# Performance work log

Hardware: AMD Instinct MI355X
Metric: run time of the kernel (lower is better)

The kernel has to match this reference:

```python
import jax, jax.numpy as jnp
import numpy as np

N_NODES = 50000
N_EDGES = 800000
IN_CH = 96
HID = 128
OUT_CH = 2


def _glorot(key, shape):
    lim = 1.0 / np.sqrt(shape[0])
    return jax.random.uniform(key, shape, jnp.float32, -lim, lim)


def setup_inputs() -> dict:
    key = jax.random.key(0)
    ks = jax.random.split(key, 16)
    x = jax.random.normal(ks[0], (N_NODES, IN_CH), jnp.float32)
    edge_index = jax.random.randint(ks[1], (2, N_EDGES), 0, N_NODES, jnp.int64)
    dims = [(IN_CH, HID), (HID, HID), (HID, HID // 2)]
    params = {}
    for i, (di, do) in enumerate(dims, start=1):
        params[f"Wl{i}"] = _glorot(ks[2 * i], (di, do))      # neighbor (lin_l)
        params[f"Wr{i}"] = _glorot(ks[2 * i + 1], (di, do))  # root (lin_r)
        params[f"b{i}"] = jnp.zeros((do,), jnp.float32)
    params["Wc"] = _glorot(ks[10], (HID // 2, OUT_CH))
    params["bc"] = jnp.zeros((OUT_CH,), jnp.float32)
    return {"x": x, "edge_index": edge_index, **params}


def _sage_conv(x, src, dst, Wl, Wr, b):
    # scatter-mean of source-node features into destination nodes (PyG mean aggr)
    n = x.shape[0]
    agg = jax.ops.segment_sum(x[src], dst, num_segments=n)          # [N, d]
    cnt = jax.ops.segment_sum(jnp.ones((src.shape[0], 1), x.dtype), dst, num_segments=n)
    mean = agg / jnp.maximum(cnt, 1.0)
    return mean @ Wl + x @ Wr + b


def reference(x, edge_index, Wl1, Wr1, b1, Wl2, Wr2, b2, Wl3, Wr3, b3, Wc, bc):
    src, dst = edge_index[0], edge_index[1]
    h = jax.nn.relu(_sage_conv(x, src, dst, Wl1, Wr1, b1))
    h = jax.nn.relu(_sage_conv(h, src, dst, Wl2, Wr2, b2))
    h = jax.nn.relu(_sage_conv(h, src, dst, Wl3, Wr3, b3))
    return h @ Wc + bc  # [N, 2] logits (dropout is identity at inference)
```

## Files before the change

kernel.cpp:

```cpp
#include <hip/hip_runtime.h>

#define N_NODES 50000
#define N_EDGES 800000
#define SCAN_NB ((N_NODES + 255) / 256)

#define NB_E 128
#define CH (N_EDGES / NB_E)
#define RSZ 25000
#define HALF_WORDS (RSZ / 2)

#define CVT_ITEMS  (N_NODES * 96 / 4)
#define CVT_NB  ((CVT_ITEMS + 255) / 256)
#define PACK1_NB 12
#define PACK2_NB 16
#define PACK3_NB 8
#define PREP_NB (CVT_NB + PACK1_NB + PACK2_NB + PACK3_NB)

typedef __attribute__((ext_vector_type(8))) short short8;
typedef __attribute__((ext_vector_type(8))) unsigned short ushort8;
typedef __attribute__((ext_vector_type(4))) float f32x4;

__device__ __forceinline__ float bf2f(unsigned short u) {
  unsigned int x = ((unsigned int)u) << 16;
  return __builtin_bit_cast(float, x);
}
__device__ __forceinline__ unsigned short f2bf(float f) {
  unsigned int x = __builtin_bit_cast(unsigned int, f);
  unsigned int r = x + 0x7FFFu + ((x >> 16) & 1u);
  return (unsigned short)(r >> 16);
}


__device__ __forceinline__ void pack_w_section(const float* __restrict__ Wl,
                                               const float* __restrict__ Wr,
                                               ushort* __restrict__ wcat,
                                               int K, int J2, int bid) {
  int idx = bid * 256 + threadIdx.x;
  int Jcat = 2 * J2;
  int total = (K / 8) * Jcat;
  if (idx >= total) return;
  int kk8 = idx / Jcat, j = idx % Jcat;
  const float* W = (j < J2) ? Wl : Wr;
  int jj = (j < J2) ? j : j - J2;
  ushort8 v;
  #pragma unroll
  for (int i = 0; i < 8; i++) v[i] = f2bf(W[(kk8 * 8 + i) * J2 + jj]);
  *(ushort8*)(wcat + (size_t)idx * 8) = v;
}

__global__ __launch_bounds__(256) void prep_kernel(
    const float* __restrict__ x, ushort* __restrict__ xb,
    const float* __restrict__ Wl1, const float* __restrict__ Wr1, ushort* __restrict__ wcat1,
    const float* __restrict__ Wl2, const float* __restrict__ Wr2, ushort* __restrict__ wcat2,
    const float* __restrict__ Wl3, const float* __restrict__ Wr3, ushort* __restrict__ wcat3) {
  int bid = blockIdx.x;
  if (bid < CVT_NB) {
    int i = bid * 256 + threadIdx.x;
    if (i < CVT_ITEMS) {
      f32x4 v = __builtin_nontemporal_load((const f32x4*)(x + i * 4));
      ushort4 o = make_ushort4(f2bf(v.x), f2bf(v.y), f2bf(v.z), f2bf(v.w));
      *(ushort4*)(xb + i * 4) = o;
    }
    return;
  }
  bid -= CVT_NB;
  if (bid < PACK1_NB) { pack_w_section(Wl1, Wr1, wcat1, 96, 128, bid); return; }
  bid -= PACK1_NB;
  if (bid < PACK2_NB) { pack_w_section(Wl2, Wr2, wcat2, 128, 128, bid); return; }
  bid -= PACK2_NB;
  pack_w_section(Wl3, Wr3, wcat3, 128, 64, bid);
}


__global__ __launch_bounds__(256) void hist_lds(const int* __restrict__ dst,
                                                ushort* __restrict__ hist_g) {
  __shared__ unsigned hist[HALF_WORDS];
  for (int j = threadIdx.x; j < HALF_WORDS; j += 256) hist[j] = 0;
  __syncthreads();
  int b = blockIdx.x >> 1, r = blockIdx.x & 1;
  int base = b * CH;
  for (int i = threadIdx.x; i < CH; i += 256) {
    int d = __builtin_nontemporal_load(dst + base + i);
    unsigned ld = (unsigned)(d - r * RSZ);
    if (ld < RSZ) atomicAdd(&hist[ld >> 1], (ld & 1) ? 65536u : 1u);
  }
  __syncthreads();
  unsigned* outp = (unsigned*)(hist_g + (size_t)b * N_NODES + r * RSZ);
  for (int j = threadIdx.x; j < HALF_WORDS; j += 256) outp[j] = hist[j];
}

__device__ __forceinline__ int block_excl_scan_256(int v, int tid, int* tot_out) {
  __shared__ int ws[4];
  int lane = tid & 63, wid = tid >> 6;
  int incl = v;
  #pragma unroll
  for (int off = 1; off < 64; off <<= 1) {
    int t = __shfl_up(incl, off);
    if (lane >= off) incl += t;
  }
  if (lane == 63) ws[wid] = incl;
  __syncthreads();
  int woff = 0;
  #pragma unroll
  for (int w = 0; w < 4; w++) woff += (w < wid) ? ws[w] : 0;
  *tot_out = ws[0] + ws[1] + ws[2] + ws[3];
  return woff + incl - v;
}

__global__ __launch_bounds__(256) void scanA(const ushort* __restrict__ hist_g,
                                             ushort* __restrict__ cum_g,
                                             int* __restrict__ rowptr,
                                             int* __restrict__ blocksum, int n) {
  int i = blockIdx.x * 256 + threadIdx.x;
  int run = 0;
  if (i < n) {
    for (int b = 0; b < NB_E; b++) {
      size_t o = (size_t)b * N_NODES + i;
      int c = hist_g[o];
      cum_g[o] = (ushort)run;
      run += c;
    }
  }
  int tot;
  int excl = block_excl_scan_256(run, threadIdx.x, &tot);
  if (i < n) rowptr[i] = excl;
  if (threadIdx.x == 0) blocksum[blockIdx.x] = tot;
}

__global__ __launch_bounds__(256) void scanB(const int* __restrict__ blocksum,
                                             int* __restrict__ blockoff,
                                             int* __restrict__ rowptr, int nb, int n) {
  int tid = threadIdx.x;
  int v = (tid < nb) ? blocksum[tid] : 0;
  int tot;
  int excl = block_excl_scan_256(v, tid, &tot);
  if (tid < nb) blockoff[tid] = excl;
  if (tid == 0) rowptr[n] = tot;
}

__global__ __launch_bounds__(256) void scanC(int* __restrict__ rowptr,
                                             const int* __restrict__ blockoff, int n) {
  int i = blockIdx.x * 256 + threadIdx.x;
  if (i < n) rowptr[i] += blockoff[blockIdx.x];
}

__global__ __launch_bounds__(256) void fill_lds(const int* __restrict__ src,
                                                const int* __restrict__ dst,
                                                const ushort* __restrict__ cum_g,
                                                const int* __restrict__ rowptr,
                                                ushort* __restrict__ csr) {
  __shared__ unsigned cur[HALF_WORDS];
  int b = blockIdx.x >> 1, r = blockIdx.x & 1;
  const unsigned* cg = (const unsigned*)(cum_g + (size_t)b * N_NODES + r * RSZ);
  for (int j = threadIdx.x; j < HALF_WORDS; j += 256) cur[j] = cg[j];
  __syncthreads();
  int base = b * CH;
  for (int i = threadIdx.x; i < CH; i += 256) {
    int d = __builtin_nontemporal_load(dst + base + i);
    int s = __builtin_nontemporal_load(src + base + i);
    unsigned ld = (unsigned)(d - r * RSZ);
    if (ld < RSZ) {
      unsigned old = atomicAdd(&cur[ld >> 1], (ld & 1) ? 65536u : 1u);
      unsigned loc = (ld & 1) ? (old >> 16) : (old & 0xffffu);
      csr[(size_t)rowptr[d] + loc] = (ushort)s;
    }
  }
}

template <int K, int J2>
__global__ __launch_bounds__(256) void gemm_mfma(
    const ushort* __restrict__ hb, const ushort* __restrict__ wcat,
    ushort* __restrict__ tl, ushort* __restrict__ tr, int n) {
  constexpr int Jcat = 2 * J2;
  constexpr int NT = Jcat / 16;
  constexpr int KS = K / 32;
  constexpr int BM = 128;
  constexpr int LDS_US = (BM * Jcat > K * Jcat) ? BM * Jcat : K * Jcat;
  __shared__ ushort lds[LDS_US];

  int tid = threadIdx.x;
  int wid = tid >> 6, lane = tid & 63;
  int row0 = blockIdx.x * BM;

  constexpr int WCH = K * Jcat / 8;
  for (int c = tid; c < WCH; c += 256) {
    *(ushort8*)(lds + c * 8) = *(const ushort8*)(wcat + (size_t)c * 8);
  }
  __syncthreads();

  int rg = lane >> 4, lc = lane & 15;
  int r0 = row0 + wid * 32 + lc;
  int r1 = r0 + 16;
  long ar0 = (long)min(r0, n - 1) * K;
  long ar1 = (long)min(r1, n - 1) * K;

  f32x4 acc[2][NT];
  #pragma unroll
  for (int mt = 0; mt < 2; mt++)
    #pragma unroll
    for (int jt = 0; jt < NT; jt++) acc[mt][jt] = (f32x4){0.f, 0.f, 0.f, 0.f};

  #pragma unroll
  for (int ks = 0; ks < KS; ks++) {
    int koff = ks * 32 + rg * 8;
    short8 a0 = *(const short8*)(hb + ar0 + koff);
    short8 a1 = *(const short8*)(hb + ar1 + koff);
    int kk8 = ks * 4 + rg;
    #pragma unroll
    for (int jt = 0; jt < NT; jt++) {
      short8 bfr = *(const short8*)(lds + ((size_t)kk8 * Jcat + jt * 16 + lc) * 8);
      acc[0][jt] = __builtin_amdgcn_mfma_f32_16x16x32_bf16(a0, bfr, acc[0][jt], 0, 0, 0);
      acc[1][jt] = __builtin_amdgcn_mfma_f32_16x16x32_bf16(a1, bfr, acc[1][jt], 0, 0, 0);
    }
  }
  __syncthreads();

  #pragma unroll
  for (int mt = 0; mt < 2; mt++) {
    int rbase = wid * 32 + mt * 16 + rg * 4;
    #pragma unroll
    for (int jt = 0; jt < NT; jt++) {
      int col = jt * 16 + lc;
      #pragma unroll
      for (int r = 0; r < 4; r++)
        lds[(size_t)(rbase + r) * Jcat + col] = f2bf(acc[mt][jt][r]);
    }
  }
  __syncthreads();

  constexpr int CPR = J2 / 8;
  for (int i = tid; i < BM * 2 * CPR; i += 256) {
    int row = i / (2 * CPR), cc = i % (2 * CPR);
    int grow = row0 + row;
    if (grow < n) {
      ushort8 v = *(ushort8*)(lds + (size_t)row * Jcat + cc * 8);
      ushort* dstp = (cc < CPR) ? (tl + (size_t)grow * J2 + cc * 8)
                                : (tr + (size_t)grow * J2 + (size_t)(cc - CPR) * 8);
      *(ushort8*)dstp = v;
    }
  }
}

__global__ __launch_bounds__(256) void agg_relu128(
    const ushort* __restrict__ tl, const ushort* __restrict__ tr,
    const float* __restrict__ bias,
    const int* __restrict__ rowptr, const ushort* __restrict__ csr,
    ushort* __restrict__ hout, int n) {
  int node = blockIdx.x * 16 + (threadIdx.x >> 4);
  int lane = threadIdx.x & 15;
  if (node >= n) return;
  int lo = rowptr[node], hi = rowptr[node + 1];

  float s[8];
  #pragma unroll
  for (int i = 0; i < 8; i++) s[i] = 0.f;

  int e = lo;
  for (; e + 1 < hi; e += 2) {
    int i0 = csr[e], i1 = csr[e + 1];
    ushort8 v0 = *(const ushort8*)(tl + (size_t)i0 * 128 + lane * 8);
    ushort8 v1 = *(const ushort8*)(tl + (size_t)i1 * 128 + lane * 8);
    #pragma unroll
    for (int i = 0; i < 8; i++) s[i] += bf2f(v0[i]) + bf2f(v1[i]);
  }
  if (e < hi) {
    int i0 = csr[e];
    ushort8 v0 = *(const ushort8*)(tl + (size_t)i0 * 128 + lane * 8);
    #pragma unroll
    for (int i = 0; i < 8; i++) s[i] += bf2f(v0[i]);
  }

  int deg = hi - lo;
  float inv = (deg > 0) ? 1.f / (float)deg : 0.f;
  ushort8 tv = *(const ushort8*)(tr + (size_t)node * 128 + lane * 8);
  float4 b0 = *(const float4*)(bias + lane * 8);
  float4 b1 = *(const float4*)(bias + lane * 8 + 4);
  float bb[8] = {b0.x, b0.y, b0.z, b0.w, b1.x, b1.y, b1.z, b1.w};
  ushort8 o;
  #pragma unroll
  for (int i = 0; i < 8; i++) {
    float v = s[i] * inv + bf2f(tv[i]) + bb[i];
    o[i] = f2bf(v > 0.f ? v : 0.f);
  }
  *(ushort8*)(hout + (size_t)node * 128 + lane * 8) = o;
}

__global__ __launch_bounds__(256) void agg_head(
    const ushort* __restrict__ tl, const ushort* __restrict__ tr,
    const float* __restrict__ bias, const float* __restrict__ Wc,
    const float* __restrict__ bc,
    const int* __restrict__ rowptr, const ushort* __restrict__ csr,
    float* __restrict__ out, int n) {
  int node = blockIdx.x * 32 + (threadIdx.x >> 3);
  int lane = threadIdx.x & 7;
  if (node >= n) return;
  int lo = rowptr[node], hi = rowptr[node + 1];

  float s[8];
  #pragma unroll
  for (int i = 0; i < 8; i++) s[i] = 0.f;

  int e = lo;
  for (; e + 1 < hi; e += 2) {
    int i0 = csr[e], i1 = csr[e + 1];
    ushort8 v0 = *(const ushort8*)(tl + (size_t)i0 * 64 + lane * 8);
    ushort8 v1 = *(const ushort8*)(tl + (size_t)i1 * 64 + lane * 8);
    #pragma unroll
    for (int i = 0; i < 8; i++) s[i] += bf2f(v0[i]) + bf2f(v1[i]);
  }
  if (e < hi) {
    int i0 = csr[e];
    ushort8 v0 = *(const ushort8*)(tl + (size_t)i0 * 64 + lane * 8);
    #pragma unroll
    for (int i = 0; i < 8; i++) s[i] += bf2f(v0[i]);
  }

  int deg = hi - lo;
  float inv = (deg > 0) ? 1.f / (float)deg : 0.f;
  ushort8 tv = *(const ushort8*)(tr + (size_t)node * 64 + lane * 8);
  float p0 = 0.f, p1 = 0.f;
  #pragma unroll
  for (int i = 0; i < 8; i++) {
    int k = lane * 8 + i;
    float v = s[i] * inv + bf2f(tv[i]) + bias[k];
    v = v > 0.f ? v : 0.f;
    p0 += v * Wc[k * 2 + 0];
    p1 += v * Wc[k * 2 + 1];
  }
  #pragma unroll
  for (int off = 1; off < 8; off <<= 1) {
    p0 += __shfl_xor(p0, off);
    p1 += __shfl_xor(p1, off);
  }
  if (lane == 0) {
    out[(size_t)node * 2 + 0] = p0 + bc[0];
    out[(size_t)node * 2 + 1] = p1 + bc[1];
  }
}

extern "C" void kernel_launch(void* const* d_in, const int* in_sizes, int n_in,
                              void* d_out, int out_size, void* d_ws, size_t ws_size,
                              hipStream_t stream) {
  const float* x   = (const float*)d_in[0];
  const int*   ei  = (const int*)d_in[1];
  const float* Wl1 = (const float*)d_in[2];
  const float* Wr1 = (const float*)d_in[3];
  const float* b1  = (const float*)d_in[4];
  const float* Wl2 = (const float*)d_in[5];
  const float* Wr2 = (const float*)d_in[6];
  const float* b2  = (const float*)d_in[7];
  const float* Wl3 = (const float*)d_in[8];
  const float* Wr3 = (const float*)d_in[9];
  const float* b3  = (const float*)d_in[10];
  const float* Wc  = (const float*)d_in[11];
  const float* bc  = (const float*)d_in[12];
  float* out = (float*)d_out;

  const int* src = ei;
  const int* dst = ei + N_EDGES;

  char* ws = (char*)d_ws;
  size_t off = 0;
  auto alloc = [&](size_t bytes) -> void* {
    void* p = ws + off;
    off += (bytes + 255) & ~(size_t)255;
    return p;
  };
  int*    rowptr   = (int*)alloc((N_NODES + 1) * sizeof(int));
  ushort* csr      = (ushort*)alloc(N_EDGES * sizeof(ushort));
  int*    blocksum = (int*)alloc(256 * sizeof(int));
  int*    blockoff = (int*)alloc(256 * sizeof(int));
  ushort* xb       = (ushort*)alloc((size_t)N_NODES * 96 * 2);
  ushort* wcat1    = (ushort*)alloc((size_t)96 * 256 * 2);
  ushort* wcat2    = (ushort*)alloc((size_t)128 * 256 * 2);
  ushort* wcat3    = (ushort*)alloc((size_t)128 * 128 * 2);
  ushort* tl       = (ushort*)alloc((size_t)N_NODES * 128 * 2);
  ushort* tr       = (ushort*)alloc((size_t)N_NODES * 128 * 2);
  ushort* hA       = (ushort*)alloc((size_t)N_NODES * 128 * 2);
  ushort* hB       = (ushort*)alloc((size_t)N_NODES * 128 * 2);
  (void)ws_size; (void)n_in; (void)in_sizes; (void)out_size;

  ushort* hist_g = tl;
  ushort* cum_g  = tr;

  prep_kernel<<<PREP_NB, 256, 0, stream>>>(x, xb,
                                           Wl1, Wr1, wcat1,
                                           Wl2, Wr2, wcat2,
                                           Wl3, Wr3, wcat3);

  hist_lds<<<NB_E * 2, 256, 0, stream>>>(dst, hist_g);
  scanA<<<SCAN_NB, 256, 0, stream>>>(hist_g, cum_g, rowptr, blocksum, N_NODES);
  scanB<<<1, 256, 0, stream>>>(blocksum, blockoff, rowptr, SCAN_NB, N_NODES);
  scanC<<<SCAN_NB, 256, 0, stream>>>(rowptr, blockoff, N_NODES);
  fill_lds<<<NB_E * 2, 256, 0, stream>>>(src, dst, cum_g, rowptr, csr);

  const int gemm_grid = (N_NODES + 127) / 128;
  const int agg_grid  = (N_NODES + 15) / 16;
  const int head_grid = (N_NODES + 31) / 32;

  gemm_mfma<96, 128><<<gemm_grid, 256, 0, stream>>>(xb, wcat1, tl, tr, N_NODES);
  agg_relu128<<<agg_grid, 256, 0, stream>>>(tl, tr, b1, rowptr, csr, hA, N_NODES);
  gemm_mfma<128, 128><<<gemm_grid, 256, 0, stream>>>(hA, wcat2, tl, tr, N_NODES);
  agg_relu128<<<agg_grid, 256, 0, stream>>>(tl, tr, b2, rowptr, csr, hB, N_NODES);
  gemm_mfma<128, 64><<<gemm_grid, 256, 0, stream>>>(hB, wcat3, tl, tr, N_NODES);
  agg_head<<<head_grid, 256, 0, stream>>>(tl, tr, b3, Wc, bc, rowptr, csr, out, N_NODES);
}
```

Baseline: 195.3 us.

## Fuse scan passes, read GEMM weights from global, unroll gather by eight

Merges the two small scan kernels into one, where each block recomputes the block-offset scan and applies its own offset, removing a launch. The GEMM no longer stages weights in LDS and writes outputs straight from the accumulators with scalar stores, dropping barriers and the staging pass at the cost of uncoalesced 2-byte stores and repeated global/L2 weight reads. The aggregation kernels add an eight-edge unrolled gather so more neighbour loads are in flight at once.

```diff
diff --git a/kernel.cpp b/kernel.cpp
--- a/kernel.cpp
+++ b/kernel.cpp
@@ -127,21 +127,19 @@
   if (threadIdx.x == 0) blocksum[blockIdx.x] = tot;
 }
 
-__global__ __launch_bounds__(256) void scanB(const int* __restrict__ blocksum,
-                                             int* __restrict__ blockoff,
-                                             int* __restrict__ rowptr, int nb, int n) {
+__global__ __launch_bounds__(256) void scanBC(const int* __restrict__ blocksum,
+                                              int* __restrict__ rowptr, int n) {
+  __shared__ int exls[256];
   int tid = threadIdx.x;
-  int v = (tid < nb) ? blocksum[tid] : 0;
+  int v = (tid < SCAN_NB) ? blocksum[tid] : 0;
   int tot;
   int excl = block_excl_scan_256(v, tid, &tot);
-  if (tid < nb) blockoff[tid] = excl;
-  if (tid == 0) rowptr[n] = tot;
-}
-
-__global__ __launch_bounds__(256) void scanC(int* __restrict__ rowptr,
-                                             const int* __restrict__ blockoff, int n) {
-  int i = blockIdx.x * 256 + threadIdx.x;
-  if (i < n) rowptr[i] += blockoff[blockIdx.x];
+  exls[tid] = excl;
+  __syncthreads();
+  int myoff = exls[blockIdx.x];
+  int i = blockIdx.x * 256 + tid;
+  if (i < n) rowptr[i] += myoff;
+  if (blockIdx.x == 0 && tid == 0) rowptr[n] = tot;
 }
 
 __global__ __launch_bounds__(256) void fill_lds(const int* __restrict__ src,
@@ -174,21 +172,11 @@
   constexpr int Jcat = 2 * J2;
   constexpr int NT = Jcat / 16;
   constexpr int KS = K / 32;
-  constexpr int BM = 128;
-  constexpr int LDS_US = (BM * Jcat > K * Jcat) ? BM * Jcat : K * Jcat;
-  __shared__ ushort lds[LDS_US];
 
   int tid = threadIdx.x;
   int wid = tid >> 6, lane = tid & 63;
-  int row0 = blockIdx.x * BM;
-
-  constexpr int WCH = K * Jcat / 8;
-  for (int c = tid; c < WCH; c += 256) {
-    *(ushort8*)(lds + c * 8) = *(const ushort8*)(wcat + (size_t)c * 8);
-  }
-  __syncthreads();
-
   int rg = lane >> 4, lc = lane & 15;
+  int row0 = blockIdx.x * 128;
   int r0 = row0 + wid * 32 + lc;
   int r1 = r0 + 16;
   long ar0 = (long)min(r0, n - 1) * K;
@@ -208,12 +196,11 @@
     int kk8 = ks * 4 + rg;
     #pragma unroll
     for (int jt = 0; jt < NT; jt++) {
-      short8 bfr = *(const short8*)(lds + ((size_t)kk8 * Jcat + jt * 16 + lc) * 8);
+      short8 bfr = *(const short8*)(wcat + ((size_t)kk8 * Jcat + jt * 16 + lc) * 8);
       acc[0][jt] = __builtin_amdgcn_mfma_f32_16x16x32_bf16(a0, bfr, acc[0][jt], 0, 0, 0);
       acc[1][jt] = __builtin_amdgcn_mfma_f32_16x16x32_bf16(a1, bfr, acc[1][jt], 0, 0, 0);
     }
   }
-  __syncthreads();
 
   #pragma unroll
   for (int mt = 0; mt < 2; mt++) {
@@ -221,22 +208,13 @@
     #pragma unroll
     for (int jt = 0; jt < NT; jt++) {
       int col = jt * 16 + lc;
+      ushort* outp = (col < J2) ? tl : tr;
+      int cm = (col < J2) ? col : col - J2;
       #pragma unroll
-      for (int r = 0; r < 4; r++)
-        lds[(size_t)(rbase + r) * Jcat + col] = f2bf(acc[mt][jt][r]);
-    }
-  }
-  __syncthreads();
-
-  constexpr int CPR = J2 / 8;
-  for (int i = tid; i < BM * 2 * CPR; i += 256) {
-    int row = i / (2 * CPR), cc = i % (2 * CPR);
-    int grow = row0 + row;
-    if (grow < n) {
-      ushort8 v = *(ushort8*)(lds + (size_t)row * Jcat + cc * 8);
-      ushort* dstp = (cc < CPR) ? (tl + (size_t)grow * J2 + cc * 8)
-                                : (tr + (size_t)grow * J2 + (size_t)(cc - CPR) * 8);
-      *(ushort8*)dstp = v;
+      for (int r = 0; r < 4; r++) {
+        int grow = row0 + rbase + r;
+        if (grow < n) outp[(size_t)grow * J2 + cm] = f2bf(acc[mt][jt][r]);
+      }
     }
   }
 }
@@ -250,22 +228,30 @@
   int lane = threadIdx.x & 15;
   if (node >= n) return;
   int lo = rowptr[node], hi = rowptr[node + 1];
+  const ushort* tb = tl + lane * 8;
 
   float s[8];
   #pragma unroll
   for (int i = 0; i < 8; i++) s[i] = 0.f;
 
   int e = lo;
+  for (; e + 7 < hi; e += 8) {
+    ushort8 v[8];
+    #pragma unroll
+    for (int q = 0; q < 8; q++) v[q] = *(const ushort8*)(tb + (size_t)csr[e + q] * 128);
+    #pragma unroll
+    for (int q = 0; q < 8; q++)
+      #pragma unroll
+      for (int i = 0; i < 8; i++) s[i] += bf2f(v[q][i]);
+  }
   for (; e + 1 < hi; e += 2) {
-    int i0 = csr[e], i1 = csr[e + 1];
-    ushort8 v0 = *(const ushort8*)(tl + (size_t)i0 * 128 + lane * 8);
-    ushort8 v1 = *(const ushort8*)(tl + (size_t)i1 * 128 + lane * 8);
+    ushort8 v0 = *(const ushort8*)(tb + (size_t)csr[e] * 128);
+    ushort8 v1 = *(const ushort8*)(tb + (size_t)csr[e + 1] * 128);
     #pragma unroll
     for (int i = 0; i < 8; i++) s[i] += bf2f(v0[i]) + bf2f(v1[i]);
   }
   if (e < hi) {
-    int i0 = csr[e];
-    ushort8 v0 = *(const ushort8*)(tl + (size_t)i0 * 128 + lane * 8);
+    ushort8 v0 = *(const ushort8*)(tb + (size_t)csr[e] * 128);
     #pragma unroll
     for (int i = 0; i < 8; i++) s[i] += bf2f(v0[i]);
   }
@@ -295,22 +281,30 @@
   int lane = threadIdx.x & 7;
   if (node >= n) return;
   int lo = rowptr[node], hi = rowptr[node + 1];
+  const ushort* tb = tl + lane * 8;
 
   float s[8];
   #pragma unroll
   for (int i = 0; i < 8; i++) s[i] = 0.f;
 
   int e = lo;
+  for (; e + 7 < hi; e += 8) {
+    ushort8 v[8];
+    #pragma unroll
+    for (int q = 0; q < 8; q++) v[q] = *(const ushort8*)(tb + (size_t)csr[e + q] * 64);
+    #pragma unroll
+    for (int q = 0; q < 8; q++)
+      #pragma unroll
+      for (int i = 0; i < 8; i++) s[i] += bf2f(v[q][i]);
+  }
   for (; e + 1 < hi; e += 2) {
-    int i0 = csr[e], i1 = csr[e + 1];
-    ushort8 v0 = *(const ushort8*)(tl + (size_t)i0 * 64 + lane * 8);
-    ushort8 v1 = *(const ushort8*)(tl + (size_t)i1 * 64 + lane * 8);
+    ushort8 v0 = *(const ushort8*)(tb + (size_t)csr[e] * 64);
+    ushort8 v1 = *(const ushort8*)(tb + (size_t)csr[e + 1] * 64);
     #pragma unroll
     for (int i = 0; i < 8; i++) s[i] += bf2f(v0[i]) + bf2f(v1[i]);
   }
   if (e < hi) {
-    int i0 = csr[e];
-    ushort8 v0 = *(const ushort8*)(tl + (size_t)i0 * 64 + lane * 8);
+    ushort8 v0 = *(const ushort8*)(tb + (size_t)csr[e] * 64);
     #pragma unroll
     for (int i = 0; i < 8; i++) s[i] += bf2f(v0[i]);
   }
@@ -369,7 +363,6 @@
   int*    rowptr   = (int*)alloc((N_NODES + 1) * sizeof(int));
   ushort* csr      = (ushort*)alloc(N_EDGES * sizeof(ushort));
   int*    blocksum = (int*)alloc(256 * sizeof(int));
-  int*    blockoff = (int*)alloc(256 * sizeof(int));
   ushort* xb       = (ushort*)alloc((size_t)N_NODES * 96 * 2);
   ushort* wcat1    = (ushort*)alloc((size_t)96 * 256 * 2);
   ushort* wcat2    = (ushort*)alloc((size_t)128 * 256 * 2);
@@ -390,8 +383,7 @@
 
   hist_lds<<<NB_E * 2, 256, 0, stream>>>(dst, hist_g);
   scanA<<<SCAN_NB, 256, 0, stream>>>(hist_g, cum_g, rowptr, blocksum, N_NODES);
-  scanB<<<1, 256, 0, stream>>>(blocksum, blockoff, rowptr, SCAN_NB, N_NODES);
-  scanC<<<SCAN_NB, 256, 0, stream>>>(rowptr, blockoff, N_NODES);
+  scanBC<<<SCAN_NB, 256, 0, stream>>>(blocksum, rowptr, N_NODES);
   fill_lds<<<NB_E * 2, 256, 0, stream>>>(src, dst, cum_g, rowptr, csr);
 
   const int gemm_grid = (N_NODES + 127) / 128;
```

After: 198.7 us. About the same (+1.7%).
